# Kernel tuning notes

Hardware: AMD Instinct MI355X
Metric: run time of the kernel (lower is better)

Reference implementation:

```python
import jax, jax.numpy as jnp
import numpy as np

D = 1152      # model dim
E = 4         # num_experts
HID = 768     # llama FFN hidden: multiple_of*ceil(int(2*1152/3)/256)
NH = 8        # cross-attention heads
TEMP = 2.0    # expert gumbel temperature (eval: no decay)


def _gumbel_softmax(key, logits, temp, hard):
    g = jax.random.gumbel(key, logits.shape, logits.dtype)
    y = jax.nn.softmax((logits + g) / temp, axis=-1)
    if hard:
        oh = jax.nn.one_hot(jnp.argmax(y, axis=-1), logits.shape[-1], dtype=logits.dtype)
        y = oh - jax.lax.stop_gradient(y) + y
    return y


def _mha(x, mem, in_w, in_b, out_w, out_b):
    # torch nn.MultiheadAttention(batch_first=True): packed qkv in_proj.
    B, S, Dm = x.shape
    hd = Dm // NH
    q = x @ in_w[:Dm].T + in_b[:Dm]
    k = mem @ in_w[Dm:2 * Dm].T + in_b[Dm:2 * Dm]
    v = mem @ in_w[2 * Dm:].T + in_b[2 * Dm:]
    q = q.reshape(B, S, NH, hd).transpose(0, 2, 1, 3)
    k = k.reshape(B, -1, NH, hd).transpose(0, 2, 1, 3)
    v = v.reshape(B, -1, NH, hd).transpose(0, 2, 1, 3)
    a = jax.nn.softmax(jnp.einsum('bhqd,bhkd->bhqk', q, k) / jnp.sqrt(jnp.asarray(hd, x.dtype)), axis=-1)
    o = jnp.einsum('bhqk,bhkd->bhqd', a, v).transpose(0, 2, 1, 3).reshape(B, S, Dm)
    return o @ out_w.T + out_b


def _ff_all(x2d, w1, w2, w3):
    # all E llama SwiGLU experts densely: x2d [N,D], w1/w3 [E,HID,D], w2 [E,D,HID] -> [N,E,D]
    h1 = jnp.einsum('nd,ehd->neh', x2d, w1)
    h3 = jnp.einsum('nd,ehd->neh', x2d, w3)
    return jnp.einsum('neh,edh->ned', jax.nn.silu(h1) * h3, w2)


def setup_inputs() -> dict:
    key = jax.random.key(0)
    ks = jax.random.split(key, 32)
    s = 0.02
    B, S, Sc = 2, 1024, 128
    inp = {
        'x': jax.random.normal(ks[0], (B, S, D), jnp.float32),
        'time': jax.random.normal(ks[1], (B, D), jnp.float32),
        'caption': jax.random.normal(ks[2], (B, Sc, D), jnp.float32),
        'acoustic': jax.random.normal(ks[3], (B, S, D), jnp.float32),
        'attn_in_w': jax.random.normal(ks[4], (3 * D, D), jnp.float32) * s,
        'attn_in_b': jnp.zeros((3 * D,), jnp.float32),
        'attn_out_w': jax.random.normal(ks[5], (D, D), jnp.float32) * s,
        'attn_out_b': jnp.zeros((D,), jnp.float32),
        'hl_w': jax.random.normal(ks[6], (2, D), jnp.float32) * s,
        'hl_b': jnp.zeros((2,), jnp.float32),
        'cap_gate_w': jax.random.normal(ks[7], (E, D), jnp.float32) * s,
        'cap_gate_b': jnp.zeros((E,), jnp.float32),
        'ac_gate_w': jax.random.normal(ks[8], (E, D), jnp.float32) * s,
        'ac_gate_b': jnp.zeros((E,), jnp.float32),
        'cap_w1': jax.random.normal(ks[9], (E, HID, D), jnp.float32) * s,
        'cap_w2': jax.random.normal(ks[10], (E, D, HID), jnp.float32) * s,
        'cap_w3': jax.random.normal(ks[11], (E, HID, D), jnp.float32) * s,
        'ac_w1': jax.random.normal(ks[12], (E, HID, D), jnp.float32) * s,
        'ac_w2': jax.random.normal(ks[13], (E, D, HID), jnp.float32) * s,
        'ac_w3': jax.random.normal(ks[14], (E, HID, D), jnp.float32) * s,
        'fr_w1': jax.random.normal(ks[15], (E, HID, D), jnp.float32) * s,
        'fr_w2': jax.random.normal(ks[16], (E, D, HID), jnp.float32) * s,
        'fr_w3': jax.random.normal(ks[17], (E, HID, D), jnp.float32) * s,
    }
    return inp


def reference(x, time, caption, acoustic,
              attn_in_w, attn_in_b, attn_out_w, attn_out_b,
              hl_w, hl_b, cap_gate_w, cap_gate_b, ac_gate_w, ac_gate_b,
              cap_w1, cap_w2, cap_w3, ac_w1, ac_w2, ac_w3,
              fr_w1, fr_w2, fr_w3):
    B, S, Dm = x.shape
    # cross-attention: x attends over caption, output replaces caption stream
    ca = _mha(x, caption, attn_in_w, attn_in_b, attn_out_w, attn_out_b)
    cap2 = ca.reshape(-1, Dm)          # [N, D]
    x2 = x.reshape(-1, Dm)             # [N, D]
    ac2 = acoustic.reshape(-1, Dm)     # [N, D]
    # high-level caption/acoustic gate from time embedding, broadcast over tokens
    hl = jnp.repeat(time @ hl_w.T + hl_b, S, axis=0)  # [N, 2]
    k1, k2, k3 = jax.random.split(jax.random.key(42), 3)
    hp = _gumbel_softmax(k1, hl, 1.0, False)
    cm = hp[:, 0:1]   # caption mask [N,1]
    am = hp[:, 1:2]   # acoustic mask [N,1]
    # expert gates (eval: hard one-hot straight-through)
    cp = _gumbel_softmax(k2, cap2 @ cap_gate_w.T + cap_gate_b, TEMP, True)  # [N,E]
    ap = _gumbel_softmax(k3, ac2 @ ac_gate_w.T + ac_gate_b, TEMP, True)    # [N,E]
    # dense per-expert SwiGLU, masked combine
    zc = jnp.einsum('ned,ne->nd', _ff_all(x2, cap_w1, cap_w2, cap_w3), cp) * cm
    za = jnp.einsum('ned,ne->nd', _ff_all(x2, ac_w1, ac_w2, ac_w3), ap) * am
    y = (zc + za).reshape(B, S, Dm)
    # frequency experts: each expert sees y masked to its channel block, keeps its block
    r = Dm // E
    region = ((jnp.arange(Dm)[None, :] // r) == jnp.arange(E)[:, None]).astype(x.dtype)  # [E,D]
    ym = y[None] * region[:, None, None, :]  # [E,B,S,D]
    h1 = jnp.einsum('ebsd,ehd->ebsh', ym, fr_w1)
    h3 = jnp.einsum('ebsd,ehd->ebsh', ym, fr_w3)
    fo = jnp.einsum('ebsh,edh->ebsd', jax.nn.silu(h1) * h3, fr_w2)  # [E,B,S,D]
    z = jnp.concatenate([fo[e, :, :, e * r:(e + 1) * r] for e in range(E)], axis=-1)
    # load balancing loss
    probs = jnp.concatenate([cp, ap], axis=1)                                  # [N,2E]
    masks = jnp.concatenate([jnp.tile(cm, (1, E)), jnp.tile(am, (1, E))], axis=1)
    usage = (probs * masks).sum(axis=0) / (masks.sum() + 1e-10)
    lb_loss = jnp.mean(usage * jnp.log(usage + 1e-10))
    return z, lb_loss
```

## Files before the change

kernel.cpp:

```cpp
#include <hip/hip_runtime.h>
#include <stdint.h>

#define NDIM 1152
#define NEXP 4
#define NHID 768
#define NHEAD 8
#define HDIM 144
#define NB 2
#define NS 1024
#define NSC 128
#define NTOK 2048
#define NCAP 256

typedef _Float16 f16;
typedef _Float16 f16x4 __attribute__((ext_vector_type(4)));
typedef _Float16 f16x8 __attribute__((ext_vector_type(8)));
typedef float f32x4 __attribute__((ext_vector_type(4)));

#define MFMA16(a, b, c) __builtin_amdgcn_mfma_f32_16x16x32_f16(a, b, c, 0, 0, 0)

#define WSZ ((size_t)NEXP * NHID * NDIM)
#define WQ  ((size_t)(WSZ / 4))
#define OFF_CW2 ((size_t)4 * WSZ)
#define OFF_AW2 ((size_t)5 * WSZ)
#define OFF_FR1 ((size_t)6 * WSZ)
#define OFF_FR3 ((size_t)6 * WSZ + WQ)
#define OFF_FR2 ((size_t)6 * WSZ + 2 * WQ)

__device__ inline uint2 tfry(uint32_t k0, uint32_t k1, uint32_t x0, uint32_t x1) {
  uint32_t k2 = k0 ^ k1 ^ 0x1BD11BDAu;
#define RND(r) { x0 += x1; x1 = (x1 << r) | (x1 >> (32 - r)); x1 ^= x0; }
  x0 += k0; x1 += k1;
  RND(13) RND(15) RND(26) RND(6)
  x0 += k1; x1 += k2 + 1u;
  RND(17) RND(29) RND(16) RND(24)
  x0 += k2; x1 += k0 + 2u;
  RND(13) RND(15) RND(26) RND(6)
  x0 += k0; x1 += k1 + 3u;
  RND(17) RND(29) RND(16) RND(24)
  x0 += k1; x1 += k2 + 4u;
  RND(13) RND(15) RND(26) RND(6)
  x0 += k2; x1 += k0 + 5u;
#undef RND
  return make_uint2(x0, x1);
}

__device__ inline float b2g(uint32_t bits) {
  uint32_t fb = (bits >> 9) | 0x3f800000u;
  float f = __uint_as_float(fb) - 1.0f;
  const float tiny = 1.1754943508222875e-38f;
  float u = f * 1.0f + tiny;
  u = fmaxf(tiny, u);
  return -logf(-logf(u));
}

__global__ void k_prep(const float* __restrict__ timep, const float* __restrict__ hlw,
                       const float* __restrict__ hlb,
                       float* __restrict__ g1, float* __restrict__ g2, float* __restrict__ g3,
                       float* __restrict__ tl) {
  int t = threadIdx.x;
  uint2 k1 = tfry(0u, 42u, 0u, 0u);
  uint2 k2 = tfry(0u, 42u, 0u, 1u);
  uint2 k3 = tfry(0u, 42u, 0u, 2u);
  for (int p = t; p < 4096; p += 256) {
    uint2 o = tfry(k1.x, k1.y, 0u, (uint32_t)p);
    g1[p] = b2g(o.x ^ o.y);
  }
  for (int p = t; p < 8192; p += 256) {
    uint2 o2 = tfry(k2.x, k2.y, 0u, (uint32_t)p);
    g2[p] = b2g(o2.x ^ o2.y);
    uint2 o3 = tfry(k3.x, k3.y, 0u, (uint32_t)p);
    g3[p] = b2g(o3.x ^ o3.y);
  }
  int wv = t >> 6, lane = t & 63;
  {
    int b = wv >> 1, j = wv & 1;
    float s = 0.f;
    for (int k = lane; k < NDIM; k += 64) s += timep[b * NDIM + k] * hlw[j * NDIM + k];
    for (int m = 32; m; m >>= 1) s += __shfl_xor(s, m);
    if (lane == 0) tl[b * 2 + j] = s + hlb[j];
  }
}

__global__ void k_fuse_gate1(const float* __restrict__ ow, const float* __restrict__ gw,
                             float* __restrict__ wpp) {
  int kt = blockIdx.x % 5;
  int dc = blockIdx.x / 5;
  int k = kt * 256 + threadIdx.x;
  if (k >= NDIM) return;
  float a0 = 0.f, a1 = 0.f, a2 = 0.f, a3 = 0.f;
#pragma unroll 8
  for (int j = 0; j < 64; ++j) {
    int d = dc * 64 + j;
    float o = ow[(size_t)d * NDIM + k];
    a0 += gw[d] * o;
    a1 += gw[NDIM + d] * o;
    a2 += gw[2 * NDIM + d] * o;
    a3 += gw[3 * NDIM + d] * o;
  }
  float* p = wpp + (size_t)dc * 4 * NDIM;
  p[k] = a0; p[NDIM + k] = a1; p[2 * NDIM + k] = a2; p[3 * NDIM + k] = a3;
}

__global__ void k_fuse_gate2(const float* __restrict__ wpp,
                             const float* __restrict__ gw, const float* __restrict__ ob,
                             const float* __restrict__ gb,
                             float* __restrict__ wp, float* __restrict__ bp) {
  if (blockIdx.x == 18) {
    int wv = threadIdx.x >> 6, lane = threadIdx.x & 63;
    float s = 0.f;
    for (int d = lane; d < NDIM; d += 64) s += ob[d] * gw[wv * NDIM + d];
    for (int m = 32; m; m >>= 1) s += __shfl_xor(s, m);
    if (lane == 0) bp[wv] = s + gb[wv];
    return;
  }
  int i = blockIdx.x * 256 + threadIdx.x;
  float s = 0.f;
#pragma unroll
  for (int c = 0; c < 18; ++c) s += wpp[(size_t)c * 4 * NDIM + i];
  wp[i] = s;
}

__global__ void k_ac_logits(const float* __restrict__ ac, const float* __restrict__ agw,
                            const float* __restrict__ agb, float* __restrict__ al) {
  int wv = threadIdx.x >> 6, lane = threadIdx.x & 63;
  int n = blockIdx.x * 4 + wv;
  float s[NEXP] = {0.f, 0.f, 0.f, 0.f};
  for (int d = lane; d < NDIM; d += 64) {
    float a = ac[(size_t)n * NDIM + d];
#pragma unroll
    for (int e = 0; e < NEXP; ++e) s[e] += a * agw[e * NDIM + d];
  }
#pragma unroll
  for (int e = 0; e < NEXP; ++e)
    for (int m = 32; m; m >>= 1) s[e] += __shfl_xor(s[e], m);
  if (lane == 0) {
#pragma unroll
    for (int e = 0; e < NEXP; ++e) al[n * NEXP + e] = s[e] + agb[e];
  }
}

__global__ void k_o_logits(const f16* __restrict__ ohi, const f16* __restrict__ olo,
                           const float* __restrict__ wp, const float* __restrict__ bp,
                           float* __restrict__ cl) {
  int wv = threadIdx.x >> 6, lane = threadIdx.x & 63;
  int n = blockIdx.x * 4 + wv;
  float s[NEXP] = {0.f, 0.f, 0.f, 0.f};
  for (int d = lane; d < NDIM; d += 64) {
    size_t gi = (size_t)n * NDIM + d;
    float a = (float)ohi[gi] + (float)olo[gi] * (1.f / 2048.f);
#pragma unroll
    for (int e = 0; e < NEXP; ++e) s[e] += a * wp[e * NDIM + d];
  }
#pragma unroll
  for (int e = 0; e < NEXP; ++e)
    for (int m = 32; m; m >>= 1) s[e] += __shfl_xor(s[e], m);
  if (lane == 0) {
#pragma unroll
    for (int e = 0; e < NEXP; ++e) cl[n * NEXP + e] = s[e] + bp[e];
  }
}

__global__ void k_cvt_split(const float* __restrict__ src, f16* __restrict__ hi,
                            f16* __restrict__ lo, int n) {
  int i = (blockIdx.x * 256 + threadIdx.x) * 4;
  if (i + 3 < n) {
    float4 v = *(const float4*)(src + i);
    f16x4 h, l;
    h[0] = (f16)v.x; l[0] = (f16)((v.x - (float)h[0]) * 2048.f);
    h[1] = (f16)v.y; l[1] = (f16)((v.y - (float)h[1]) * 2048.f);
    h[2] = (f16)v.z; l[2] = (f16)((v.z - (float)h[2]) * 2048.f);
    h[3] = (f16)v.w; l[3] = (f16)((v.w - (float)h[3]) * 2048.f);
    *(f16x4*)(hi + i) = h;
    *(f16x4*)(lo + i) = l;
  }
}

__global__ __launch_bounds__(256) void k_gemm_qkv(
    const f16* __restrict__ xhi, const f16* __restrict__ xlo,
    const f16* __restrict__ caphi, const f16* __restrict__ caplo,
    const float* __restrict__ inw, const float* __restrict__ inb,
    f16* __restrict__ qhi, f16* __restrict__ qlo,
    f16* __restrict__ khi, f16* __restrict__ klo,
    f16* __restrict__ vthi, f16* __restrict__ vtlo,
    const float* __restrict__ w0, const float* __restrict__ w1,
    const float* __restrict__ w2, const float* __restrict__ w3,
    f16* __restrict__ wf16) {
  int z = blockIdx.z;
  if (z >= 3) {
    int cvtid = (z - 3) * 576 + blockIdx.y * 18 + blockIdx.x;
    size_t c0 = (size_t)cvtid * 12288;
    int slot = (int)(c0 / WSZ);
    size_t base = c0 % WSZ;
    const float* s = ((slot == 0) ? w0 : (slot == 1) ? w1 : (slot == 2) ? w2 : w3) + base;
    f16* dst = wf16 + (size_t)slot * WSZ + base;
#pragma unroll
    for (int i = 0; i < 6; ++i) {
      size_t off = (size_t)(threadIdx.x + i * 256) * 8;
      float4 v0 = *(const float4*)(s + off);
      float4 v1 = *(const float4*)(s + off + 4);
      f16x8 h;
      h[0] = (f16)v0.x; h[1] = (f16)v0.y; h[2] = (f16)v0.z; h[3] = (f16)v0.w;
      h[4] = (f16)v1.x; h[5] = (f16)v1.y; h[6] = (f16)v1.z; h[7] = (f16)v1.w;
      *(f16x8*)(dst + off) = h;
    }
    return;
  }
  int M = (z == 0) ? NTOK : NCAP;
  int mt = blockIdx.y, nt = blockIdx.x;
  if (mt * 64 >= M) return;
  const f16* Ah_g = (z == 0) ? xhi : caphi;
  const f16* Al_g = (z == 0) ? xlo : caplo;
  __shared__ f16 Ash[64 * 72];
  __shared__ f16 Asl[64 * 72];
  __shared__ f16 Bsh[64 * 72];
  __shared__ f16 Bsl[64 * 72];
  int t = threadIdx.x;
  int wv = t >> 6, lane = t & 63, m16 = lane & 15, quad = lane >> 4;
  int r0 = t >> 3, ak = (t & 7) * 8;
  size_t a0o = (size_t)(mt * 64 + r0) * NDIM;
  size_t a1o = (size_t)(mt * 64 + r0 + 32) * NDIM;
  f32x4 zf = {0.f, 0.f, 0.f, 0.f};
  f32x4 ah[2][2] = {{zf, zf}, {zf, zf}};
  f32x4 am[2][2] = {{zf, zf}, {zf, zf}};
  uint4 rah0, rah1, ral0, ral1;
  float4 rbw[4];
  rah0 = *(const uint4*)(Ah_g + a0o + ak);
  rah1 = *(const uint4*)(Ah_g + a1o + ak);
  ral0 = *(const uint4*)(Al_g + a0o + ak);
  ral1 = *(const uint4*)(Al_g + a1o + ak);
#pragma unroll
  for (int uu = 0; uu < 4; ++uu) {
    int u = t + uu * 256;
    int rr = u >> 4, kp = (u & 15) * 4;
    rbw[uu] = *(const float4*)(inw + (size_t)(z * NDIM + nt * 64 + rr) * NDIM + kp);
  }
  for (int kc = 0; kc < NDIM; kc += 64) {
    __syncthreads();
    *(uint4*)&Ash[r0 * 72 + ak] = rah0;
    *(uint4*)&Ash[(r0 + 32) * 72 + ak] = rah1;
    *(uint4*)&Asl[r0 * 72 + ak] = ral0;
    *(uint4*)&Asl[(r0 + 32) * 72 + ak] = ral1;
#pragma unroll
    for (int uu = 0; uu < 4; ++uu) {
      int u = t + uu * 256;
      int rr = u >> 4, kp = (u & 15) * 4;
      f16x4 hb, lb;
      hb[0] = (f16)rbw[uu].x; lb[0] = (f16)((rbw[uu].x - (float)hb[0]) * 2048.f);
      hb[1] = (f16)rbw[uu].y; lb[1] = (f16)((rbw[uu].y - (float)hb[1]) * 2048.f);
      hb[2] = (f16)rbw[uu].z; lb[2] = (f16)((rbw[uu].z - (float)hb[2]) * 2048.f);
      hb[3] = (f16)rbw[uu].w; lb[3] = (f16)((rbw[uu].w - (float)hb[3]) * 2048.f);
      *(f16x4*)&Bsh[rr * 72 + kp] = hb;
      *(f16x4*)&Bsl[rr * 72 + kp] = lb;
    }
    __syncthreads();
    int kn = kc + 64;
    if (kn < NDIM) {
      rah0 = *(const uint4*)(Ah_g + a0o + kn + ak);
      rah1 = *(const uint4*)(Ah_g + a1o + kn + ak);
      ral0 = *(const uint4*)(Al_g + a0o + kn + ak);
      ral1 = *(const uint4*)(Al_g + a1o + kn + ak);
#pragma unroll
      for (int uu = 0; uu < 4; ++uu) {
        int u = t + uu * 256;
        int rr = u >> 4, kp = (u & 15) * 4;
        rbw[uu] = *(const float4*)(inw + (size_t)(z * NDIM + nt * 64 + rr) * NDIM + kn + kp);
      }
    }
#pragma unroll
    for (int ks = 0; ks < 2; ++ks) {
      int aoff = ((wv & 1) * 32 + m16) * 72 + ks * 32 + quad * 8;
      int boff = ((wv >> 1) * 32 + m16) * 72 + ks * 32 + quad * 8;
      f16x8 a0h = *(const f16x8*)&Ash[aoff];
      f16x8 a1h = *(const f16x8*)&Ash[aoff + 16 * 72];
      f16x8 a0l = *(const f16x8*)&Asl[aoff];
      f16x8 a1l = *(const f16x8*)&Asl[aoff + 16 * 72];
      f16x8 b0h = *(const f16x8*)&Bsh[boff];
      f16x8 b1h = *(const f16x8*)&Bsh[boff + 16 * 72];
      f16x8 b0l = *(const f16x8*)&Bsl[boff];
      f16x8 b1l = *(const f16x8*)&Bsl[boff + 16 * 72];
      ah[0][0] = MFMA16(a0h, b0h, ah[0][0]);
      ah[0][1] = MFMA16(a0h, b1h, ah[0][1]);
      ah[1][0] = MFMA16(a1h, b0h, ah[1][0]);
      ah[1][1] = MFMA16(a1h, b1h, ah[1][1]);
      am[0][0] = MFMA16(a0h, b0l, am[0][0]);
      am[0][1] = MFMA16(a0h, b1l, am[0][1]);
      am[1][0] = MFMA16(a1h, b0l, am[1][0]);
      am[1][1] = MFMA16(a1h, b1l, am[1][1]);
      am[0][0] = MFMA16(a0l, b0h, am[0][0]);
      am[0][1] = MFMA16(a0l, b1h, am[0][1]);
      am[1][0] = MFMA16(a1l, b0h, am[1][0]);
      am[1][1] = MFMA16(a1l, b1h, am[1][1]);
    }
  }
#pragma unroll
  for (int mi = 0; mi < 2; ++mi)
#pragma unroll
    for (int ni = 0; ni < 2; ++ni)
#pragma unroll
      for (int r = 0; r < 4; ++r) {
        int row = mt * 64 + (wv & 1) * 32 + mi * 16 + quad * 4 + r;
        int col = nt * 64 + (wv >> 1) * 32 + ni * 16 + m16;
        float v = ah[mi][ni][r] + am[mi][ni][r] * (1.f / 2048.f) + inb[z * NDIM + col];
        size_t idx = (size_t)row * NDIM + col;
        if (z == 0) {
          f16 hq = (f16)v;
          qhi[idx] = hq;
          qlo[idx] = (f16)((v - (float)hq) * 2048.f);
        } else if (z == 1) {
          f16 hk = (f16)v;
          khi[idx] = hk;
          klo[idx] = (f16)((v - (float)hk) * 2048.f);
        } else {
          f16 hv = (f16)v;
          int bb = row >> 7, kv = row & 127;
          size_t ti = (size_t)(bb * NDIM + col) * NSC + kv;
          vthi[ti] = hv;
          vtlo[ti] = (f16)((v - (float)hv) * 2048.f);
        }
      }
}

__global__ __launch_bounds__(256) void k_attn(
    const f16* __restrict__ qhi, const f16* __restrict__ qlo,
    const f16* __restrict__ khi, const f16* __restrict__ klo,
    const f16* __restrict__ vthi, const f16* __restrict__ vtlo,
    f16* __restrict__ ohi, f16* __restrict__ olo) {
  int mt = blockIdx.x, bh = blockIdx.y;
  int b = bh >> 3, h = bh & 7;
  __shared__ f16 Ah[64 * 160];
  __shared__ f16 Al[64 * 160];
  __shared__ f16 Bh[32 * 160];
  __shared__ f16 Bl[32 * 160];
  __shared__ f16 Ph[64 * 136];
  __shared__ f16 Pl[64 * 136];
  int t = threadIdx.x;
  int wv = t >> 6, lane = t & 63, m16 = lane & 15, quad = lane >> 4;
  for (int u = t; u < 64 * 20; u += 256) {
    int r = u / 20, kp = (u % 20) * 8;
    uint4 vh = make_uint4(0u, 0u, 0u, 0u), vl = vh;
    if (kp < HDIM) {
      size_t gi = (size_t)(b * NS + mt * 64 + r) * NDIM + h * HDIM + kp;
      vh = *(const uint4*)&qhi[gi];
      vl = *(const uint4*)&qlo[gi];
    }
    *(uint4*)&Ah[r * 160 + kp] = vh;
    *(uint4*)&Al[r * 160 + kp] = vl;
  }
  __syncthreads();
  f16x8 ahf[5], alf[5];
#pragma unroll
  for (int ks = 0; ks < 5; ++ks) {
    int ao = (wv * 16 + m16) * 160 + ks * 32 + quad * 8;
    ahf[ks] = *(const f16x8*)&Ah[ao];
    alf[ks] = *(const f16x8*)&Al[ao];
  }
  f32x4 zf = {0.f, 0.f, 0.f, 0.f};
  f32x4 sh_[4][2], sm_[4][2];
#pragma unroll
  for (int kt = 0; kt < 4; ++kt)
#pragma unroll
    for (int ni = 0; ni < 2; ++ni) { sh_[kt][ni] = zf; sm_[kt][ni] = zf; }
  for (int kt = 0; kt < 4; ++kt) {
    if (kt) __syncthreads();
    for (int u = t; u < 32 * 20; u += 256) {
      int r = u / 20, kp = (u % 20) * 8;
      uint4 vh = make_uint4(0u, 0u, 0u, 0u), vl = vh;
      if (kp < HDIM) {
        size_t gi = (size_t)(b * NSC + kt * 32 + r) * NDIM + h * HDIM + kp;
        vh = *(const uint4*)&khi[gi];
        vl = *(const uint4*)&klo[gi];
      }
      *(uint4*)&Bh[r * 160 + kp] = vh;
      *(uint4*)&Bl[r * 160 + kp] = vl;
    }
    __syncthreads();
#pragma unroll
    for (int ks = 0; ks < 5; ++ks) {
#pragma unroll
      for (int ni = 0; ni < 2; ++ni) {
        int bo = (ni * 16 + m16) * 160 + ks * 32 + quad * 8;
        f16x8 bhf = *(const f16x8*)&Bh[bo];
        f16x8 blf = *(const f16x8*)&Bl[bo];
        sh_[kt][ni] = MFMA16(ahf[ks], bhf, sh_[kt][ni]);
        sm_[kt][ni] = MFMA16(ahf[ks], blf, sm_[kt][ni]);
        sm_[kt][ni] = MFMA16(alf[ks], bhf, sm_[kt][ni]);
      }
    }
  }
  float sv[4][2][4];
  float mx[4] = {-1e30f, -1e30f, -1e30f, -1e30f};
#pragma unroll
  for (int kt = 0; kt < 4; ++kt)
#pragma unroll
    for (int ni = 0; ni < 2; ++ni)
#pragma unroll
      for (int r = 0; r < 4; ++r) {
        float s = (sh_[kt][ni][r] + sm_[kt][ni][r] * (1.f / 2048.f)) * (1.f / 12.f);
        sv[kt][ni][r] = s;
        mx[r] = fmaxf(mx[r], s);
      }
#pragma unroll
  for (int r = 0; r < 4; ++r) {
    mx[r] = fmaxf(mx[r], __shfl_xor(mx[r], 1));
    mx[r] = fmaxf(mx[r], __shfl_xor(mx[r], 2));
    mx[r] = fmaxf(mx[r], __shfl_xor(mx[r], 4));
    mx[r] = fmaxf(mx[r], __shfl_xor(mx[r], 8));
  }
  float sum[4] = {0.f, 0.f, 0.f, 0.f};
#pragma unroll
  for (int kt = 0; kt < 4; ++kt)
#pragma unroll
    for (int ni = 0; ni < 2; ++ni)
#pragma unroll
      for (int r = 0; r < 4; ++r) {
        float e = expf(sv[kt][ni][r] - mx[r]);
        sv[kt][ni][r] = e;
        sum[r] += e;
      }
  float inv[4];
// ... 406 lines not shown
    __syncthreads();
    int kn = kc + 64;
    if (kn < NHID) {
      ra0 = *(const uint4*)(ar0 + kn + ak);
      ra1 = *(const uint4*)(ar1 + kn + ak);
      rb0 = *(const uint4*)(br0 + kn + ak);
      rb1 = *(const uint4*)(br1 + kn + ak);
    }
#pragma unroll
    for (int ks = 0; ks < 2; ++ks) {
      int aoff = ((wv & 1) * 32 + m16) * 72 + ks * 32 + quad * 8;
      int boff = ((wv >> 1) * 32 + m16) * 72 + ks * 32 + quad * 8;
      f16x8 a0 = *(const f16x8*)&As[aoff];
      f16x8 a1 = *(const f16x8*)&As[aoff + 16 * 72];
      f16x8 b0 = *(const f16x8*)&Bs[boff];
      f16x8 b1 = *(const f16x8*)&Bs[boff + 16 * 72];
      acc[0][0] = MFMA16(a0, b0, acc[0][0]);
      acc[0][1] = MFMA16(a0, b1, acc[0][1]);
      acc[1][0] = MFMA16(a1, b0, acc[1][0]);
      acc[1][1] = MFMA16(a1, b1, acc[1][1]);
    }
  }
#pragma unroll
  for (int mi = 0; mi < 2; ++mi)
#pragma unroll
    for (int ni = 0; ni < 2; ++ni)
#pragma unroll
      for (int r = 0; r < 4; ++r) {
        int mg = mt * 64 + (wv & 1) * 32 + mi * 16 + quad * 4 + r;
        if (mg < cnt) {
          int tok = list[mg];
          int col = nt * 64 + (wv >> 1) * 32 + ni * 16 + m16;
          float v = acc[mi][ni][r] * sc[tok];
          y[(size_t)tok * NDIM + col] = v;
        }
      }
}

__global__ __launch_bounds__(256) void k_gemm2_fr(
    const f16* __restrict__ tbuf, const f16* __restrict__ wf, float* __restrict__ zz) {
  int e = blockIdx.z;
  int mt = blockIdx.y, nt = blockIdx.x;
  const f16* A = tbuf + (size_t)e * NTOK * NHID;
  const f16* Bw = wf + OFF_FR2 + (size_t)e * 288 * NHID;
  int t = threadIdx.x;
  int wv = t >> 6, lane = t & 63, m16 = lane & 15, quad = lane >> 4;
  int r0 = t >> 3, ak = (t & 7) * 8;
  const f16* ar0 = A + (size_t)(mt * 64 + r0) * NHID;
  const f16* ar1 = A + (size_t)(mt * 64 + r0 + 32) * NHID;
  int ne0 = min(nt * 64 + r0, 287), ne1 = min(nt * 64 + r0 + 32, 287);
  const f16* br0 = Bw + (size_t)ne0 * NHID;
  const f16* br1 = Bw + (size_t)ne1 * NHID;
  __shared__ f16 As[64 * 72];
  __shared__ f16 Bs[64 * 72];
  f32x4 zf = {0.f, 0.f, 0.f, 0.f};
  f32x4 acc[2][2] = {{zf, zf}, {zf, zf}};
  uint4 ra0, ra1, rb0, rb1;
  ra0 = *(const uint4*)(ar0 + ak);
  ra1 = *(const uint4*)(ar1 + ak);
  rb0 = *(const uint4*)(br0 + ak);
  rb1 = *(const uint4*)(br1 + ak);
  for (int kc = 0; kc < NHID; kc += 64) {
    __syncthreads();
    *(uint4*)&As[r0 * 72 + ak] = ra0;
    *(uint4*)&As[(r0 + 32) * 72 + ak] = ra1;
    *(uint4*)&Bs[r0 * 72 + ak] = rb0;
    *(uint4*)&Bs[(r0 + 32) * 72 + ak] = rb1;
    __syncthreads();
    int kn = kc + 64;
    if (kn < NHID) {
      ra0 = *(const uint4*)(ar0 + kn + ak);
      ra1 = *(const uint4*)(ar1 + kn + ak);
      rb0 = *(const uint4*)(br0 + kn + ak);
      rb1 = *(const uint4*)(br1 + kn + ak);
    }
#pragma unroll
    for (int ks = 0; ks < 2; ++ks) {
      int aoff = ((wv & 1) * 32 + m16) * 72 + ks * 32 + quad * 8;
      int boff = ((wv >> 1) * 32 + m16) * 72 + ks * 32 + quad * 8;
      f16x8 a0 = *(const f16x8*)&As[aoff];
      f16x8 a1 = *(const f16x8*)&As[aoff + 16 * 72];
      f16x8 b0 = *(const f16x8*)&Bs[boff];
      f16x8 b1 = *(const f16x8*)&Bs[boff + 16 * 72];
      acc[0][0] = MFMA16(a0, b0, acc[0][0]);
      acc[0][1] = MFMA16(a0, b1, acc[0][1]);
      acc[1][0] = MFMA16(a1, b0, acc[1][0]);
      acc[1][1] = MFMA16(a1, b1, acc[1][1]);
    }
  }
#pragma unroll
  for (int mi = 0; mi < 2; ++mi)
#pragma unroll
    for (int ni = 0; ni < 2; ++ni)
#pragma unroll
      for (int r = 0; r < 4; ++r) {
        int cg = nt * 64 + (wv >> 1) * 32 + ni * 16 + m16;
        if (cg < 288) {
          int row = mt * 64 + (wv & 1) * 32 + mi * 16 + quad * 4 + r;
          zz[(size_t)row * NDIM + e * 288 + cg] = acc[mi][ni][r];
        }
      }
}

extern "C" void kernel_launch(void* const* d_in, const int* in_sizes, int n_in,
                              void* d_out, int out_size, void* d_ws, size_t ws_size,
                              hipStream_t stream) {
  const float* x          = (const float*)d_in[0];
  const float* timep      = (const float*)d_in[1];
  const float* caption    = (const float*)d_in[2];
  const float* acoustic   = (const float*)d_in[3];
  const float* attn_in_w  = (const float*)d_in[4];
  const float* attn_in_b  = (const float*)d_in[5];
  const float* attn_out_w = (const float*)d_in[6];
  const float* attn_out_b = (const float*)d_in[7];
  const float* hl_w       = (const float*)d_in[8];
  const float* hl_b       = (const float*)d_in[9];
  const float* cap_gate_w = (const float*)d_in[10];
  const float* cap_gate_b = (const float*)d_in[11];
  const float* ac_gate_w  = (const float*)d_in[12];
  const float* ac_gate_b  = (const float*)d_in[13];
  const float* cap_w1     = (const float*)d_in[14];
  const float* cap_w2     = (const float*)d_in[15];
  const float* cap_w3     = (const float*)d_in[16];
  const float* ac_w1      = (const float*)d_in[17];
  const float* ac_w2      = (const float*)d_in[18];
  const float* ac_w3      = (const float*)d_in[19];
  const float* fr_w1      = (const float*)d_in[20];
  const float* fr_w2      = (const float*)d_in[21];
  const float* fr_w3      = (const float*)d_in[22];
  (void)in_sizes; (void)n_in; (void)out_size; (void)ws_size;

  float* zout = (float*)d_out;
  float* loss = zout + (size_t)NTOK * NDIM;

  char* wsb = (char*)d_ws;
  size_t off = 0;
  auto alloc = [&](size_t bytes) -> void* {
    void* p = wsb + off;
    off = (off + bytes + 255) & ~(size_t)255;
    return p;
  };
  float* g1     = (float*)alloc(4096 * 4);
  float* g2     = (float*)alloc(8192 * 4);
  float* g3     = (float*)alloc(8192 * 4);
  float* tl     = (float*)alloc(4 * 4);
  float* al     = (float*)alloc((size_t)NTOK * NEXP * 4);
  float* cl     = (float*)alloc((size_t)NTOK * NEXP * 4);
  float* cmv    = (float*)alloc((size_t)NTOK * 4);
  float* amv    = (float*)alloc((size_t)NTOK * 4);
  int*   lists  = (int*)alloc((size_t)8 * NTOK * 4);
  int*   counts = (int*)alloc(8 * 4);
  float* wp     = (float*)alloc((size_t)NEXP * NDIM * 4);
  float* bp     = (float*)alloc(NEXP * 4);
  float* wpp    = (float*)alloc((size_t)18 * NEXP * NDIM * 4);
  f16*   xhi    = (f16*)alloc((size_t)NTOK * NDIM * 2);
  f16*   wf16   = (f16*)alloc((size_t)(6 * WSZ + 3 * WQ) * 2);
  size_t region = off;
  f16*   xlo    = (f16*)alloc((size_t)NTOK * NDIM * 2);
  f16*   caphi  = (f16*)alloc((size_t)NCAP * NDIM * 2);
  f16*   caplo  = (f16*)alloc((size_t)NCAP * NDIM * 2);
  f16*   qhi    = (f16*)alloc((size_t)NTOK * NDIM * 2);
  f16*   qlo    = (f16*)alloc((size_t)NTOK * NDIM * 2);
  f16*   khi    = (f16*)alloc((size_t)NCAP * NDIM * 2);
  f16*   klo    = (f16*)alloc((size_t)NCAP * NDIM * 2);
  f16*   vthi   = (f16*)alloc((size_t)NB * NDIM * NSC * 2);
  f16*   vtlo   = (f16*)alloc((size_t)NB * NDIM * NSC * 2);
  f16*   ohi    = (f16*)alloc((size_t)NTOK * NDIM * 2);
  f16*   olo    = (f16*)alloc((size_t)NTOK * NDIM * 2);
  off = region;
  f16*   tbuf   = (f16*)alloc((size_t)8 * NTOK * NHID * 2);
  float* ybc    = (float*)alloc((size_t)NTOK * NDIM * 4);
  float* yba    = (float*)alloc((size_t)NTOK * NDIM * 4);

  k_prep<<<dim3(1), dim3(256), 0, stream>>>(timep, hl_w, hl_b, g1, g2, g3, tl);
  k_fuse_gate1<<<dim3(90), dim3(256), 0, stream>>>(attn_out_w, cap_gate_w, wpp);
  k_fuse_gate2<<<dim3(19), dim3(256), 0, stream>>>(wpp, cap_gate_w, attn_out_b,
                                                   cap_gate_b, wp, bp);
  k_ac_logits<<<dim3(512), dim3(256), 0, stream>>>(acoustic, ac_gate_w, ac_gate_b, al);
  k_cvt_split<<<dim3(2304), dim3(256), 0, stream>>>(x, xhi, xlo, NTOK * NDIM);
  k_cvt_split<<<dim3(288), dim3(256), 0, stream>>>(caption, caphi, caplo, NCAP * NDIM);
  k_gemm_qkv<<<dim3(18, 32, 5), dim3(256), 0, stream>>>(
      xhi, xlo, caphi, caplo, attn_in_w, attn_in_b,
      qhi, qlo, khi, klo, vthi, vtlo,
      cap_w1, cap_w3, ac_w1, ac_w3, wf16);
  k_attn<<<dim3(16, 16), dim3(256), 0, stream>>>(qhi, qlo, khi, klo, vthi, vtlo, ohi, olo);
  k_o_logits<<<dim3(512), dim3(256), 0, stream>>>(ohi, olo, wp, bp, cl);
  k_route<<<dim3(1), dim3(1024), 0, stream>>>(cl, al, g1, g2, g3, tl,
                                              cmv, amv, lists, counts, loss);
  k_gemm1<<<dim3(3666), dim3(256), 0, stream>>>(xhi, wf16, lists, counts, tbuf,
                                                fr_w1, fr_w3, cap_w2, ac_w2, fr_w2);
  k_gemm2<<<dim3(4608), dim3(256), 0, stream>>>(tbuf, wf16, lists, counts,
                                                cmv, amv, ybc, yba);
  k_gemm1_fr<<<dim3(12, 32, 4), dim3(256), 0, stream>>>(ybc, yba, wf16, tbuf);
  k_gemm2_fr<<<dim3(5, 32, 4), dim3(256), 0, stream>>>(tbuf, wf16, zout);
}
```

Before: 441.4 us.

## Fuse preprocessing kernels into one launch and pre-split attention input weights

Merges the gumbel/time prep, gate-weight fusion (now a single pass with a shared-memory reduction instead of a two-kernel partial sum), acoustic logits and the x/caption f16 hi/lo splits into one multi-role kernel launch. It also pre-splits attn_in_w into f16 hi/lo buffers there, so the QKV GEMM loads f16 tiles directly instead of converting fp32 weights inside every tile loop. The goal is fewer launches and less redundant conversion work, since each weight tile was previously converted once per M-tile. In exchange it adds an extra pass that writes and rereads the weight hi/lo buffers, and the single-block gumbel branch may become the slowest part of the merged launch.

```diff
diff --git a/kernel.cpp b/kernel.cpp
--- a/kernel.cpp
+++ b/kernel.cpp
@@ -26,6 +26,17 @@
 #define OFF_FR1 ((size_t)6 * WSZ)
 #define OFF_FR3 ((size_t)6 * WSZ + WQ)
 #define OFF_FR2 ((size_t)6 * WSZ + 2 * WQ)
+
+#define PRE_XB   2304
+#define PRE_CB   288
+#define PRE_IWB  1944
+#define PRE_X0   0
+#define PRE_C0   (PRE_XB)
+#define PRE_IW0  (PRE_C0 + PRE_CB)
+#define PRE_GUM  (PRE_IW0 + PRE_IWB)
+#define PRE_FG0  (PRE_GUM + 1)
+#define PRE_AL0  (PRE_FG0 + 19)
+#define PRE_NB   (PRE_AL0 + 512)
 
 __device__ inline uint2 tfry(uint32_t k0, uint32_t k1, uint32_t x0, uint32_t x1) {
   uint32_t k2 = k0 ^ k1 ^ 0x1BD11BDAu;
@@ -54,89 +65,133 @@
   return -logf(-logf(u));
 }
 
-__global__ void k_prep(const float* __restrict__ timep, const float* __restrict__ hlw,
-                       const float* __restrict__ hlb,
-                       float* __restrict__ g1, float* __restrict__ g2, float* __restrict__ g3,
-                       float* __restrict__ tl) {
+__global__ __launch_bounds__(256) void k_pre(
+    const float* __restrict__ x, const float* __restrict__ caption,
+    const float* __restrict__ inw,
+    const float* __restrict__ timep, const float* __restrict__ hlw,
+    const float* __restrict__ hlb,
+    const float* __restrict__ acous, const float* __restrict__ agw,
+    const float* __restrict__ agb,
+    const float* __restrict__ ow, const float* __restrict__ ob,
+    const float* __restrict__ gw, const float* __restrict__ gb,
+    f16* __restrict__ xhi, f16* __restrict__ xlo,
+    f16* __restrict__ caphi, f16* __restrict__ caplo,
+    f16* __restrict__ inwhi, f16* __restrict__ inwlo,
+    float* __restrict__ g1, float* __restrict__ g2, float* __restrict__ g3,
+    float* __restrict__ tl, float* __restrict__ al,
+    float* __restrict__ wp, float* __restrict__ bp) {
+  __shared__ float sm[4][4][64];
+  int bid = blockIdx.x;
   int t = threadIdx.x;
-  uint2 k1 = tfry(0u, 42u, 0u, 0u);
-  uint2 k2 = tfry(0u, 42u, 0u, 1u);
-  uint2 k3 = tfry(0u, 42u, 0u, 2u);
-  for (int p = t; p < 4096; p += 256) {
-    uint2 o = tfry(k1.x, k1.y, 0u, (uint32_t)p);
-    g1[p] = b2g(o.x ^ o.y);
-  }
-  for (int p = t; p < 8192; p += 256) {
-    uint2 o2 = tfry(k2.x, k2.y, 0u, (uint32_t)p);
-    g2[p] = b2g(o2.x ^ o2.y);
-    uint2 o3 = tfry(k3.x, k3.y, 0u, (uint32_t)p);
-    g3[p] = b2g(o3.x ^ o3.y);
-  }
-  int wv = t >> 6, lane = t & 63;
-  {
+  if (bid < PRE_C0) {
+    int i = bid * 1024 + t * 4;
+    float4 v = *(const float4*)(x + i);
+    f16x4 h, l;
+    h[0] = (f16)v.x; l[0] = (f16)((v.x - (float)h[0]) * 2048.f);
+    h[1] = (f16)v.y; l[1] = (f16)((v.y - (float)h[1]) * 2048.f);
+    h[2] = (f16)v.z; l[2] = (f16)((v.z - (float)h[2]) * 2048.f);
+    h[3] = (f16)v.w; l[3] = (f16)((v.w - (float)h[3]) * 2048.f);
+    *(f16x4*)(xhi + i) = h;
+    *(f16x4*)(xlo + i) = l;
+    return;
+  }
+  if (bid < PRE_IW0) {
+    int i = (bid - PRE_C0) * 1024 + t * 4;
+    float4 v = *(const float4*)(caption + i);
+    f16x4 h, l;
+    h[0] = (f16)v.x; l[0] = (f16)((v.x - (float)h[0]) * 2048.f);
+    h[1] = (f16)v.y; l[1] = (f16)((v.y - (float)h[1]) * 2048.f);
+    h[2] = (f16)v.z; l[2] = (f16)((v.z - (float)h[2]) * 2048.f);
+    h[3] = (f16)v.w; l[3] = (f16)((v.w - (float)h[3]) * 2048.f);
+    *(f16x4*)(caphi + i) = h;
+    *(f16x4*)(caplo + i) = l;
+    return;
+  }
+  if (bid < PRE_GUM) {
+    size_t i = (size_t)(bid - PRE_IW0) * 2048 + (size_t)t * 8;
+    float4 v0 = *(const float4*)(inw + i);
+    float4 v1 = *(const float4*)(inw + i + 4);
+    f16x8 h, l;
+    h[0] = (f16)v0.x; l[0] = (f16)((v0.x - (float)h[0]) * 2048.f);
+    h[1] = (f16)v0.y; l[1] = (f16)((v0.y - (float)h[1]) * 2048.f);
+    h[2] = (f16)v0.z; l[2] = (f16)((v0.z - (float)h[2]) * 2048.f);
+    h[3] = (f16)v0.w; l[3] = (f16)((v0.w - (float)h[3]) * 2048.f);
+    h[4] = (f16)v1.x; l[4] = (f16)((v1.x - (float)h[4]) * 2048.f);
+    h[5] = (f16)v1.y; l[5] = (f16)((v1.y - (float)h[5]) * 2048.f);
+    h[6] = (f16)v1.z; l[6] = (f16)((v1.z - (float)h[6]) * 2048.f);
+    h[7] = (f16)v1.w; l[7] = (f16)((v1.w - (float)h[7]) * 2048.f);
+    *(f16x8*)(inwhi + i) = h;
+    *(f16x8*)(inwlo + i) = l;
+    return;
+  }
+  if (bid == PRE_GUM) {
+    uint2 k1 = tfry(0u, 42u, 0u, 0u);
+    uint2 k2 = tfry(0u, 42u, 0u, 1u);
+    uint2 k3 = tfry(0u, 42u, 0u, 2u);
+    for (int p = t; p < 4096; p += 256) {
+      uint2 o = tfry(k1.x, k1.y, 0u, (uint32_t)p);
+      g1[p] = b2g(o.x ^ o.y);
+    }
+    for (int p = t; p < 8192; p += 256) {
+      uint2 o2 = tfry(k2.x, k2.y, 0u, (uint32_t)p);
+      g2[p] = b2g(o2.x ^ o2.y);
+      uint2 o3 = tfry(k3.x, k3.y, 0u, (uint32_t)p);
+      g3[p] = b2g(o3.x ^ o3.y);
+    }
+    int wv = t >> 6, lane = t & 63;
     int b = wv >> 1, j = wv & 1;
     float s = 0.f;
     for (int k = lane; k < NDIM; k += 64) s += timep[b * NDIM + k] * hlw[j * NDIM + k];
     for (int m = 32; m; m >>= 1) s += __shfl_xor(s, m);
     if (lane == 0) tl[b * 2 + j] = s + hlb[j];
-  }
-}
-
-__global__ void k_fuse_gate1(const float* __restrict__ ow, const float* __restrict__ gw,
-                             float* __restrict__ wpp) {
-  int kt = blockIdx.x % 5;
-  int dc = blockIdx.x / 5;
-  int k = kt * 256 + threadIdx.x;
-  if (k >= NDIM) return;
-  float a0 = 0.f, a1 = 0.f, a2 = 0.f, a3 = 0.f;
-#pragma unroll 8
-  for (int j = 0; j < 64; ++j) {
-    int d = dc * 64 + j;
-    float o = ow[(size_t)d * NDIM + k];
-    a0 += gw[d] * o;
-    a1 += gw[NDIM + d] * o;
-    a2 += gw[2 * NDIM + d] * o;
-    a3 += gw[3 * NDIM + d] * o;
-  }
-  float* p = wpp + (size_t)dc * 4 * NDIM;
-  p[k] = a0; p[NDIM + k] = a1; p[2 * NDIM + k] = a2; p[3 * NDIM + k] = a3;
-}
-
-__global__ void k_fuse_gate2(const float* __restrict__ wpp,
-                             const float* __restrict__ gw, const float* __restrict__ ob,
-                             const float* __restrict__ gb,
-                             float* __restrict__ wp, float* __restrict__ bp) {
-  if (blockIdx.x == 18) {
-    int wv = threadIdx.x >> 6, lane = threadIdx.x & 63;
-    float s = 0.f;
-    for (int d = lane; d < NDIM; d += 64) s += ob[d] * gw[wv * NDIM + d];
-    for (int m = 32; m; m >>= 1) s += __shfl_xor(s, m);
-    if (lane == 0) bp[wv] = s + gb[wv];
     return;
   }
-  int i = blockIdx.x * 256 + threadIdx.x;
-  float s = 0.f;
-#pragma unroll
-  for (int c = 0; c < 18; ++c) s += wpp[(size_t)c * 4 * NDIM + i];
-  wp[i] = s;
-}
-
-__global__ void k_ac_logits(const float* __restrict__ ac, const float* __restrict__ agw,
-                            const float* __restrict__ agb, float* __restrict__ al) {
-  int wv = threadIdx.x >> 6, lane = threadIdx.x & 63;
-  int n = blockIdx.x * 4 + wv;
-  float s[NEXP] = {0.f, 0.f, 0.f, 0.f};
-  for (int d = lane; d < NDIM; d += 64) {
-    float a = ac[(size_t)n * NDIM + d];
-#pragma unroll
-    for (int e = 0; e < NEXP; ++e) s[e] += a * agw[e * NDIM + d];
-  }
-#pragma unroll
-  for (int e = 0; e < NEXP; ++e)
-    for (int m = 32; m; m >>= 1) s[e] += __shfl_xor(s[e], m);
-  if (lane == 0) {
-#pragma unroll
-    for (int e = 0; e < NEXP; ++e) al[n * NEXP + e] = s[e] + agb[e];
+  if (bid < PRE_AL0) {
+    int blk = bid - PRE_FG0;
+    if (blk == 18) {
+      int wv = t >> 6, lane = t & 63;
+      float s = 0.f;
+      for (int d = lane; d < NDIM; d += 64) s += ob[d] * gw[wv * NDIM + d];
+      for (int m = 32; m; m >>= 1) s += __shfl_xor(s, m);
+      if (lane == 0) bp[wv] = s + gb[wv];
+      return;
+    }
+    int j = t & 63, w = t >> 6;
+    int k = blk * 64 + j;
+    float a0 = 0.f, a1 = 0.f, a2 = 0.f, a3 = 0.f;
+#pragma unroll 4
+    for (int d = w * 288; d < (w + 1) * 288; ++d) {
+      float o = ow[(size_t)d * NDIM + k];
+      a0 += gw[d] * o;
+      a1 += gw[NDIM + d] * o;
+      a2 += gw[2 * NDIM + d] * o;
+      a3 += gw[3 * NDIM + d] * o;
+    }
+    sm[w][0][j] = a0; sm[w][1][j] = a1; sm[w][2][j] = a2; sm[w][3][j] = a3;
+    __syncthreads();
+    if (w == 0) {
+#pragma unroll
+      for (int e = 0; e < 4; ++e)
+        wp[e * NDIM + k] = sm[0][e][j] + sm[1][e][j] + sm[2][e][j] + sm[3][e][j];
+    }
+    return;
+  }
+  {
+    int wv = t >> 6, lane = t & 63;
+    int n = (bid - PRE_AL0) * 4 + wv;
+    float s[NEXP] = {0.f, 0.f, 0.f, 0.f};
+    for (int d = lane; d < NDIM; d += 64) {
+      float a = acous[(size_t)n * NDIM + d];
+#pragma unroll
+      for (int e = 0; e < NEXP; ++e) s[e] += a * agw[e * NDIM + d];
+    }
+#pragma unroll
+    for (int e = 0; e < NEXP; ++e)
+      for (int m = 32; m; m >>= 1) s[e] += __shfl_xor(s[e], m);
+    if (lane == 0) {
+#pragma unroll
+      for (int e = 0; e < NEXP; ++e) al[n * NEXP + e] = s[e] + agb[e];
+    }
   }
 }
 
@@ -161,25 +216,11 @@
   }
 }
 
-__global__ void k_cvt_split(const float* __restrict__ src, f16* __restrict__ hi,
-                            f16* __restrict__ lo, int n) {
-  int i = (blockIdx.x * 256 + threadIdx.x) * 4;
-  if (i + 3 < n) {
-    float4 v = *(const float4*)(src + i);
-    f16x4 h, l;
-    h[0] = (f16)v.x; l[0] = (f16)((v.x - (float)h[0]) * 2048.f);
-    h[1] = (f16)v.y; l[1] = (f16)((v.y - (float)h[1]) * 2048.f);
-    h[2] = (f16)v.z; l[2] = (f16)((v.z - (float)h[2]) * 2048.f);
-    h[3] = (f16)v.w; l[3] = (f16)((v.w - (float)h[3]) * 2048.f);
-    *(f16x4*)(hi + i) = h;
-    *(f16x4*)(lo + i) = l;
-  }
-}
-
 __global__ __launch_bounds__(256) void k_gemm_qkv(
     const f16* __restrict__ xhi, const f16* __restrict__ xlo,
     const f16* __restrict__ caphi, const f16* __restrict__ caplo,
-    const float* __restrict__ inw, const float* __restrict__ inb,
+    const f16* __restrict__ inwhi, const f16* __restrict__ inwlo,
+    const float* __restrict__ inb,
     f16* __restrict__ qhi, f16* __restrict__ qlo,
     f16* __restrict__ khi, f16* __restrict__ klo,
     f16* __restrict__ vthi, f16* __restrict__ vtlo,
@@ -220,39 +261,32 @@
   int r0 = t >> 3, ak = (t & 7) * 8;
   size_t a0o = (size_t)(mt * 64 + r0) * NDIM;
   size_t a1o = (size_t)(mt * 64 + r0 + 32) * NDIM;
+  const f16* bh0 = inwhi + (size_t)(z * NDIM + nt * 64 + r0) * NDIM;
+  const f16* bh1 = bh0 + (size_t)32 * NDIM;
+  const f16* bl0 = inwlo + (size_t)(z * NDIM + nt * 64 + r0) * NDIM;
+  const f16* bl1 = bl0 + (size_t)32 * NDIM;
   f32x4 zf = {0.f, 0.f, 0.f, 0.f};
   f32x4 ah[2][2] = {{zf, zf}, {zf, zf}};
   f32x4 am[2][2] = {{zf, zf}, {zf, zf}};
-  uint4 rah0, rah1, ral0, ral1;
-  float4 rbw[4];
+  uint4 rah0, rah1, ral0, ral1, rbh0, rbh1, rbl0, rbl1;
   rah0 = *(const uint4*)(Ah_g + a0o + ak);
   rah1 = *(const uint4*)(Ah_g + a1o + ak);
   ral0 = *(const uint4*)(Al_g + a0o + ak);
   ral1 = *(const uint4*)(Al_g + a1o + ak);
-#pragma unroll
-  for (int uu = 0; uu < 4; ++uu) {
-    int u = t + uu * 256;
-    int rr = u >> 4, kp = (u & 15) * 4;
-    rbw[uu] = *(const float4*)(inw + (size_t)(z * NDIM + nt * 64 + rr) * NDIM + kp);
-  }
+  rbh0 = *(const uint4*)(bh0 + ak);
+  rbh1 = *(const uint4*)(bh1 + ak);
+  rbl0 = *(const uint4*)(bl0 + ak);
+  rbl1 = *(const uint4*)(bl1 + ak);
   for (int kc = 0; kc < NDIM; kc += 64) {
     __syncthreads();
     *(uint4*)&Ash[r0 * 72 + ak] = rah0;
     *(uint4*)&Ash[(r0 + 32) * 72 + ak] = rah1;
     *(uint4*)&Asl[r0 * 72 + ak] = ral0;
     *(uint4*)&Asl[(r0 + 32) * 72 + ak] = ral1;
-#pragma unroll
-    for (int uu = 0; uu < 4; ++uu) {
-      int u = t + uu * 256;
-      int rr = u >> 4, kp = (u & 15) * 4;
-      f16x4 hb, lb;
-      hb[0] = (f16)rbw[uu].x; lb[0] = (f16)((rbw[uu].x - (float)hb[0]) * 2048.f);
-      hb[1] = (f16)rbw[uu].y; lb[1] = (f16)((rbw[uu].y - (float)hb[1]) * 2048.f);
-      hb[2] = (f16)rbw[uu].z; lb[2] = (f16)((rbw[uu].z - (float)hb[2]) * 2048.f);
-      hb[3] = (f16)rbw[uu].w; lb[3] = (f16)((rbw[uu].w - (float)hb[3]) * 2048.f);
-      *(f16x4*)&Bsh[rr * 72 + kp] = hb;
-      *(f16x4*)&Bsl[rr * 72 + kp] = lb;
-    }
+    *(uint4*)&Bsh[r0 * 72 + ak] = rbh0;
+    *(uint4*)&Bsh[(r0 + 32) * 72 + ak] = rbh1;
+    *(uint4*)&Bsl[r0 * 72 + ak] = rbl0;
+    *(uint4*)&Bsl[(r0 + 32) * 72 + ak] = rbl1;
     __syncthreads();
     int kn = kc + 64;
     if (kn < NDIM) {
@@ -260,12 +294,10 @@
       rah1 = *(const uint4*)(Ah_g + a1o + kn + ak);
       ral0 = *(const uint4*)(Al_g + a0o + kn + ak);
       ral1 = *(const uint4*)(Al_g + a1o + kn + ak);
-#pragma unroll
-      for (int uu = 0; uu < 4; ++uu) {
-        int u = t + uu * 256;
-        int rr = u >> 4, kp = (u & 15) * 4;
-        rbw[uu] = *(const float4*)(inw + (size_t)(z * NDIM + nt * 64 + rr) * NDIM + kn + kp);
-      }
+      rbh0 = *(const uint4*)(bh0 + kn + ak);
+      rbh1 = *(const uint4*)(bh1 + kn + ak);
+      rbl0 = *(const uint4*)(bl0 + kn + ak);
+      rbl1 = *(const uint4*)(bl1 + kn + ak);
     }
 #pragma unroll
     for (int ks = 0; ks < 2; ++ks) {
@@ -978,7 +1010,6 @@
   int*   counts = (int*)alloc(8 * 4);
   float* wp     = (float*)alloc((size_t)NEXP * NDIM * 4);
   float* bp     = (float*)alloc(NEXP * 4);
-  float* wpp    = (float*)alloc((size_t)18 * NEXP * NDIM * 4);
   f16*   xhi    = (f16*)alloc((size_t)NTOK * NDIM * 2);
   f16*   wf16   = (f16*)alloc((size_t)(6 * WSZ + 3 * WQ) * 2);
   size_t region = off;
@@ -993,20 +1024,21 @@
   f16*   vtlo   = (f16*)alloc((size_t)NB * NDIM * NSC * 2);
   f16*   ohi    = (f16*)alloc((size_t)NTOK * NDIM * 2);
   f16*   olo    = (f16*)alloc((size_t)NTOK * NDIM * 2);
+  f16*   inwhi  = (f16*)alloc((size_t)3 * NDIM * NDIM * 2);
+  f16*   inwlo  = (f16*)alloc((size_t)3 * NDIM * NDIM * 2);
   off = region;
   f16*   tbuf   = (f16*)alloc((size_t)8 * NTOK * NHID * 2);
   float* ybc    = (float*)alloc((size_t)NTOK * NDIM * 4);
   float* yba    = (float*)alloc((size_t)NTOK * NDIM * 4);
 
-  k_prep<<<dim3(1), dim3(256), 0, stream>>>(timep, hl_w, hl_b, g1, g2, g3, tl);
-  k_fuse_gate1<<<dim3(90), dim3(256), 0, stream>>>(attn_out_w, cap_gate_w, wpp);
-  k_fuse_gate2<<<dim3(19), dim3(256), 0, stream>>>(wpp, cap_gate_w, attn_out_b,
-                                                   cap_gate_b, wp, bp);
-  k_ac_logits<<<dim3(512), dim3(256), 0, stream>>>(acoustic, ac_gate_w, ac_gate_b, al);
-  k_cvt_split<<<dim3(2304), dim3(256), 0, stream>>>(x, xhi, xlo, NTOK * NDIM);
-  k_cvt_split<<<dim3(288), dim3(256), 0, stream>>>(caption, caphi, caplo, NCAP * NDIM);
+  k_pre<<<dim3(PRE_NB), dim3(256), 0, stream>>>(
+      x, caption, attn_in_w, timep, hl_w, hl_b,
+      acoustic, ac_gate_w, ac_gate_b,
+      attn_out_w, attn_out_b, cap_gate_w, cap_gate_b,
+      xhi, xlo, caphi, caplo, inwhi, inwlo,
+      g1, g2, g3, tl, al, wp, bp);
   k_gemm_qkv<<<dim3(18, 32, 5), dim3(256), 0, stream>>>(
-      xhi, xlo, caphi, caplo, attn_in_w, attn_in_b,
+      xhi, xlo, caphi, caplo, inwhi, inwlo, attn_in_b,
       qhi, qlo, khi, klo, vthi, vtlo,
       cap_w1, cap_w3, ac_w1, ac_w3, wf16);
   k_attn<<<dim3(16, 16), dim3(256), 0, stream>>>(qhi, qlo, khi, klo, vthi, vtlo, ohi, olo);
```

After: 431.7 us. 2.2% less time.
